# Performance work log

Hardware: AMD Instinct MI355X
Metric: run time of the kernel (lower is better)

Reference implementation:

```python
import jax, jax.numpy as jnp
import numpy as np

B, N, C = 8, 1024, 768
HEADS = 8
HD = C // HEADS  # head_dim = qk_dim // num_heads since qk_ratio=1
SCALE = HD ** (-0.5)


def setup_inputs() -> dict:
    key = jax.random.key(0)
    ks = jax.random.split(key, 8)
    s = 0.02
    return {
        "x": jax.random.normal(ks[0], (B, N, C), dtype=jnp.float32),
        "y": jax.random.normal(ks[1], (B, N, C), dtype=jnp.float32),
        "relative_pos": jax.random.normal(ks[2], (HEADS, N, N), dtype=jnp.float32),
        "H": 32,
        "W": 32,
        "Wq": jax.random.normal(ks[3], (C, C), dtype=jnp.float32) * s,
        "Wk": jax.random.normal(ks[4], (C, C), dtype=jnp.float32) * s,
        "Wv": jax.random.normal(ks[5], (C, C), dtype=jnp.float32) * s,
        "Wp": jax.random.normal(ks[6], (C, C), dtype=jnp.float32) * s,
        "bp": jnp.zeros((C,), dtype=jnp.float32),
    }


def reference(x, y, relative_pos, H, W, Wq, Wk, Wv, Wp, bp):
    # sr_ratio == 1 path: K/V come directly from y (no spatial reduction).
    b, n, c = x.shape
    q = (x @ Wq.T).reshape(b, n, HEADS, HD)       # bnhd
    k = (y @ Wk.T).reshape(b, n, HEADS, HD)       # bmhd
    v = (y @ Wv.T).reshape(b, n, HEADS, HD)       # bmhd
    # scores: QK^T * scale + learned relative position bias (broadcast over batch)
    attn = jnp.einsum("bnhd,bmhd->bhnm", q, k) * SCALE + relative_pos[None]
    attn = jax.nn.softmax(attn, axis=-1)
    out = jnp.einsum("bhnm,bmhd->bnhd", attn, v).reshape(b, n, c)
    return out @ Wp.T + bp
```

## Files before the change

kernel.cpp:

```cpp
#include <hip/hip_runtime.h>
#include <hip/hip_bf16.h>
#include <cstdint>
#include <cstddef>


using f32x4  = __attribute__((ext_vector_type(4))) float;
using bf16x8 = __attribute__((ext_vector_type(8))) __bf16;

constexpr int Bb = 8, Nn = 1024, Cc = 768;
constexpr float LOG2E = 1.4426950408889634f;
constexpr float QSC   = 0.10206207261596575f * 1.4426950408889634f;

__device__ __forceinline__ uint16_t f2bf(float f) {
  union { float f; uint32_t u; } v; v.f = f;
  return (uint16_t)((v.u + 0x7fffu + ((v.u >> 16) & 1u)) >> 16);
}

__device__ __forceinline__ void gl_lds16(const void* g, void* l) {
  __builtin_amdgcn_global_load_lds(
      (const __attribute__((address_space(1))) void*)g,
      (__attribute__((address_space(3))) void*)l, 16, 0, 0);
}

__device__ __forceinline__ f32x4 mfma16(bf16x8 a, bf16x8 b, f32x4 c) {
  return __builtin_amdgcn_mfma_f32_16x16x32_bf16(a, b, c, 0, 0, 0);
}

template <int CTRL>
__device__ __forceinline__ float dpp_add(float v) {
  union { float f; int i; } u, r;
  u.f = v;
  r.i = __builtin_amdgcn_update_dpp(u.i, u.i, CTRL, 0xF, 0xF, false);
  return v + r.f;
}
__device__ __forceinline__ float red16_add(float v) {
  v = dpp_add<0x128>(v);
  v = dpp_add<0x124>(v);
  v = dpp_add<0x122>(v);
  v = dpp_add<0x121>(v);
  return v;
}

constexpr int NX4 = (Bb * Nn * Cc) / 4;
constexpr int NW4 = (Cc * Cc) / 4;
__global__ void cvt_all(const float* __restrict__ x, const float* __restrict__ y,
                        const float* __restrict__ wq, const float* __restrict__ wk,
                        const float* __restrict__ wv, const float* __restrict__ wp,
                        uint16_t* __restrict__ xb, uint16_t* __restrict__ yb,
                        uint16_t* __restrict__ dq, uint16_t* __restrict__ dk,
                        uint16_t* __restrict__ dv, uint16_t* __restrict__ dp) {
  int i = blockIdx.x * blockDim.x + threadIdx.x;
  const float* s; uint16_t* d; int off; float sc = 1.f;
  if (i < NX4) {
    s = x; d = xb; off = i;
  } else if (i < 2 * NX4) {
    s = y; d = yb; off = i - NX4;
  } else {
    int j = i - 2 * NX4;
    int wsel = j / NW4;
    off = j - wsel * NW4;
    switch (wsel) {
      case 0:  s = wq; d = dq; sc = QSC; break;
      case 1:  s = wk; d = dk; break;
      case 2:  s = wv; d = dv; break;
      default: s = wp; d = dp; break;
    }
  }
  float4 v = ((const float4*)s)[off];
  ushort4 o;
  o.x = f2bf(v.x * sc); o.y = f2bf(v.y * sc);
  o.z = f2bf(v.z * sc); o.w = f2bf(v.w * sc);
  ((ushort4*)d)[off] = o;
}

__device__ __forceinline__ void gemm_core(const uint16_t* __restrict__ A,
                                          const uint16_t* __restrict__ Bt,
                                          uint16_t* As, uint16_t* Bs,
                                          int m0, int n0, f32x4 (&acc)[4][4]) {
  const int tid = threadIdx.x;
  const int lane = tid & 63, l16 = lane & 15, quad = lane >> 4;
  const int w = tid >> 6;
  const int wm = (w & 1) * 64, wn = (w >> 1) * 64;

  int soff[4];
#pragma unroll
  for (int i = 0; i < 4; ++i) {
    int idx = tid + 256 * i;
    int row = idx >> 3, pc = idx & 7;
    int c = pc ^ (row & 7);
    soff[i] = row * 768 + c * 8;
  }

  for (int k0 = 0; k0 < 768; k0 += 64) {
    __syncthreads();
#pragma unroll
    for (int i = 0; i < 4; ++i)
      gl_lds16(A + (size_t)m0 * 768 + k0 + soff[i], &As[(tid + 256 * i) * 8]);
#pragma unroll
    for (int i = 0; i < 4; ++i)
      gl_lds16(Bt + (size_t)n0 * 768 + k0 + soff[i], &Bs[(tid + 256 * i) * 8]);
    __syncthreads();

#pragma unroll
    for (int ks = 0; ks < 2; ++ks) {
      bf16x8 a[4], b[4];
      const int phys = (ks * 4 + quad) ^ (l16 & 7);
#pragma unroll
      for (int i = 0; i < 4; ++i)
        a[i] = *(const bf16x8*)&As[(wm + i * 16 + l16) * 64 + phys * 8];
#pragma unroll
      for (int j = 0; j < 4; ++j)
        b[j] = *(const bf16x8*)&Bs[(wn + j * 16 + l16) * 64 + phys * 8];
#pragma unroll
      for (int i = 0; i < 4; ++i)
#pragma unroll
        for (int j = 0; j < 4; ++j)
          acc[i][j] = mfma16(a[i], b[j], acc[i][j]);
    }
  }
}

__global__ __launch_bounds__(256, 3) void qkv_kernel(
    const uint16_t* __restrict__ xb, const uint16_t* __restrict__ yb,
    const uint16_t* __restrict__ wq, const uint16_t* __restrict__ wk,
    const uint16_t* __restrict__ wv, uint16_t* __restrict__ Qb,
    uint16_t* __restrict__ Kb, uint16_t* __restrict__ Vt) {
  __shared__ uint16_t smem[128 * 130];
  const int seg = blockIdx.x / 6, nb = blockIdx.x % 6;
  const uint16_t* A  = (seg == 0) ? xb : yb;
  const uint16_t* Bt = (seg == 0) ? wq : (seg == 1) ? wk : wv;
  const int m0 = blockIdx.y * 128, n0 = nb * 128;

  f32x4 acc[4][4] = {};
  gemm_core(A, Bt, smem, smem + 8192, m0, n0, acc);

  const int tid = threadIdx.x, lane = tid & 63;
  const int l16 = lane & 15, quad = lane >> 4, w = tid >> 6;
  const int wm = (w & 1) * 64, wn = (w >> 1) * 64;

  if (seg <= 1) {
    uint16_t* O = seg ? Kb : Qb;
#pragma unroll
    for (int i = 0; i < 4; ++i)
#pragma unroll
      for (int j = 0; j < 4; ++j) {
        int col = n0 + wn + j * 16 + l16;
#pragma unroll
        for (int r = 0; r < 4; ++r) {
          int row = m0 + wm + i * 16 + quad * 4 + r;
          O[(size_t)row * 768 + col] = f2bf(acc[i][j][r]);
        }
      }
  } else {
    __syncthreads();
#pragma unroll
    for (int i = 0; i < 4; ++i)
#pragma unroll
      for (int j = 0; j < 4; ++j) {
        int ml = wm + i * 16 + quad * 4;
        int nl = wn + j * 16 + l16;
        ushort4 pk;
        pk.x = f2bf(acc[i][j][0]); pk.y = f2bf(acc[i][j][1]);
        pk.z = f2bf(acc[i][j][2]); pk.w = f2bf(acc[i][j][3]);
        *(ushort4*)&smem[nl * 130 + ml] = pk;
      }
    __syncthreads();
    const int bidx = m0 >> 10, nseq0 = m0 & 1023;
#pragma unroll
    for (int pass = 0; pass < 8; ++pass) {
      int nl = pass * 16 + (tid >> 4);
      int col = n0 + nl;
      int h = col / 96, hd = col % 96;
      int m = (tid & 15) * 8;
      bf16x8 v = *(const bf16x8*)&smem[nl * 130 + m];
      size_t o = (((size_t)(bidx * 8 + h) * 96 + hd) << 10) + nseq0 + m;
      *(bf16x8*)(Vt + o) = v;
    }
  }
}

__global__ __launch_bounds__(256, 4) void proj_kernel(
    const uint16_t* __restrict__ A, const uint16_t* __restrict__ Bt,
    float* __restrict__ out, const float* __restrict__ bias) {
  __shared__ uint16_t As[64 * 64];
  __shared__ uint16_t Bs[128 * 64];
  const int m0 = blockIdx.y * 64, n0 = blockIdx.x * 128;
  const int tid = threadIdx.x, lane = tid & 63;
  const int l16 = lane & 15, quad = lane >> 4, w = tid >> 6;
  const int wm = (w & 1) * 32, wn = (w >> 1) * 64;

  int soffA[2], soffB[4];
#pragma unroll
  for (int i = 0; i < 2; ++i) {
    int idx = tid + 256 * i;
    int row = idx >> 3, pc = idx & 7;
    soffA[i] = row * 768 + (pc ^ (row & 7)) * 8;
  }
#pragma unroll
  for (int i = 0; i < 4; ++i) {
    int idx = tid + 256 * i;
    int row = idx >> 3, pc = idx & 7;
    soffB[i] = row * 768 + (pc ^ (row & 7)) * 8;
  }

  f32x4 acc[2][4] = {};
  for (int k0 = 0; k0 < 768; k0 += 64) {
    __syncthreads();
#pragma unroll
    for (int i = 0; i < 2; ++i)
      gl_lds16(A + (size_t)m0 * 768 + k0 + soffA[i], &As[(tid + 256 * i) * 8]);
#pragma unroll
    for (int i = 0; i < 4; ++i)
      gl_lds16(Bt + (size_t)n0 * 768 + k0 + soffB[i], &Bs[(tid + 256 * i) * 8]);
    __syncthreads();
#pragma unroll
    for (int ks = 0; ks < 2; ++ks) {
      bf16x8 a[2], b[4];
      const int phys = (ks * 4 + quad) ^ (l16 & 7);
#pragma unroll
      for (int i = 0; i < 2; ++i)
        a[i] = *(const bf16x8*)&As[(wm + i * 16 + l16) * 64 + phys * 8];
#pragma unroll
      for (int j = 0; j < 4; ++j)
        b[j] = *(const bf16x8*)&Bs[(wn + j * 16 + l16) * 64 + phys * 8];
#pragma unroll
      for (int i = 0; i < 2; ++i)
#pragma unroll
        for (int j = 0; j < 4; ++j)
          acc[i][j] = mfma16(a[i], b[j], acc[i][j]);
    }
  }

  float bv[4];
#pragma unroll
  for (int j = 0; j < 4; ++j) bv[j] = bias[n0 + wn + j * 16 + l16];
#pragma unroll
  for (int i = 0; i < 2; ++i)
#pragma unroll
    for (int j = 0; j < 4; ++j) {
      int col = n0 + wn + j * 16 + l16;
#pragma unroll
      for (int r = 0; r < 4; ++r) {
        int row = m0 + wm + i * 16 + quad * 4 + r;
        out[(size_t)row * 768 + col] = acc[i][j][r] + bv[j];
      }
    }
}

__global__ __launch_bounds__(256, 2) void attn_kernel(
    const uint16_t* __restrict__ Q,
    const uint16_t* __restrict__ Kb,
    const uint16_t* __restrict__ Vt,
    const float* __restrict__ rel,
    uint16_t* __restrict__ AO) {
  __shared__ uint16_t Ks[2][64 * 96];
  __shared__ uint16_t Vs[2][96 * 64];
  __shared__ uint16_t Ps[128 * 64];

  const int tid = threadIdx.x;
  const int q0 = blockIdx.x * 128;
  const int bh = blockIdx.y;
  const int b = bh >> 3, h = bh & 7;
  const int w = tid >> 6, lane = tid & 63;
  const int l16 = lane & 15, quad = lane >> 4;
  const int l7 = l16 & 7;

  bf16x8 qf[2][3];
#pragma unroll
  for (int st = 0; st < 2; ++st) {
    const int qrow = q0 + st * 64 + w * 16 + l16;
    const uint16_t* qp =
        Q + ((size_t)(b * 1024 + qrow)) * 768 + h * 96 + quad * 8;
#pragma unroll
    for (int j = 0; j < 3; ++j) qf[st][j] = *(const bf16x8*)(qp + j * 32);
  }

  auto kSrc = [](int c) {
    int r = c / 12, pc = c % 12;
    int kc = (pc < 8) ? (pc ^ (r & 7)) : (8 + ((pc & 3) ^ (r & 3)));
    return r * 768 + kc * 8;
  };
  auto vSrc = [](int c) {
    int d = c >> 3, pc = c & 7;
    return d * 1024 + (pc ^ (d & 7)) * 8;
  };
  int koffs[3], voffs[3];
#pragma unroll
  for (int i = 0; i < 3; ++i) {
    koffs[i] = kSrc(tid + 256 * i);
    voffs[i] = vSrc(tid + 256 * i);
  }

  const uint16_t* kslab = Kb + ((size_t)(b * 1024)) * 768 + h * 96;
  const uint16_t* vslab = Vt + ((size_t)(bh * 96) << 10);
  const float* relbase0 =
      rel + ((size_t)h << 20) + ((size_t)(q0 + w * 16 + quad * 4) << 10) + l16;
  const float* relbase1 = relbase0 + (64 << 10);

  auto stage = [&](int knext, int bufi) {
    const uint16_t* kb = kslab + (size_t)knext * 768;
    const uint16_t* vb = vslab + knext;
    uint16_t* Kbuf = &Ks[bufi][0];
    uint16_t* Vbuf = &Vs[bufi][0];
#pragma unroll
    for (int i = 0; i < 3; ++i) {
      gl_lds16(kb + koffs[i], Kbuf + (tid + 256 * i) * 8);
      gl_lds16(vb + voffs[i], Vbuf + (tid + 256 * i) * 8);
    }
  };

  float relv[2][16];
  auto loadrel = [&](int knext) {
#pragma unroll
    for (int r = 0; r < 4; ++r)
#pragma unroll
      for (int nt = 0; nt < 4; ++nt) {
        relv[0][nt * 4 + r] = relbase0[(size_t)r * 1024 + knext + nt * 16];
        relv[1][nt * 4 + r] = relbase1[(size_t)r * 1024 + knext + nt * 16];
      }
  };

  float l_i[2][4] = {};
  f32x4 o_acc[2][6] = {};

  stage(0, 0);
  loadrel(0);

#pragma unroll 2
  for (int kt = 0; kt < 16; ++kt) {
    const int cur = kt & 1, nxt = (kt + 1) & 1;
    __syncthreads();
    if (kt < 15) stage((kt + 1) * 64, nxt);
    const uint16_t* KsC = &Ks[cur][0];
    const uint16_t* VsC = &Vs[cur][0];

    f32x4 s[2][4] = {};
#pragma unroll
    for (int ksi = 0; ksi < 3; ++ksi) {
#pragma unroll
      for (int nt = 0; nt < 4; ++nt) {
        const int row = nt * 16 + l16;
        const int c = ksi * 4 + quad;
        const int phys =
            (ksi < 2) ? (c ^ (row & 7)) : (8 + ((c & 3) ^ (row & 3)));
        bf16x8 kf = *(const bf16x8*)&KsC[row * 96 + phys * 8];
        s[0][nt] = mfma16(qf[0][ksi], kf, s[0][nt]);
        s[1][nt] = mfma16(qf[1][ksi], kf, s[1][nt]);
      }
    }

    const int khi = l16 >> 3;
#pragma unroll
    for (int st = 0; st < 2; ++st) {
      float pv[16];
#pragma unroll
      for (int nt = 0; nt < 4; ++nt)
#pragma unroll
        for (int r = 0; r < 4; ++r)
          pv[nt * 4 + r] = __builtin_amdgcn_exp2f(
              fmaf(relv[st][nt * 4 + r], LOG2E, s[st][nt][r]));
#pragma unroll
      for (int r = 0; r < 4; ++r)
        l_i[st][r] += (pv[r] + pv[4 + r]) + (pv[8 + r] + pv[12 + r]);
#pragma unroll
      for (int r = 0; r < 4; ++r) {
        const int qloc = quad * 4 + r;
        const int rowoff = (st * 64 + w * 16 + qloc) * 64;
        const int sw = qloc & 7;
#pragma unroll
        for (int nt = 0; nt < 4; ++nt) {
          const int kc = 2 * nt + khi;
          Ps[rowoff + (((kc ^ sw) << 3) | l7)] = f2bf(pv[nt * 4 + r]);
        }
      }
    }

    if (kt < 15) loadrel((kt + 1) * 64);

    asm volatile("s_waitcnt lgkmcnt(0)" ::: "memory");

#pragma unroll
    for (int ksi = 0; ksi < 2; ++ksi) {
      const int phys = (ksi * 4 + quad) ^ l7;
      bf16x8 pf0 = *(const bf16x8*)&Ps[(w * 16 + l16) * 64 + phys * 8];
      bf16x8 pf1 = *(const bf16x8*)&Ps[(64 + w * 16 + l16) * 64 + phys * 8];
#pragma unroll
      for (int jt = 0; jt < 6; ++jt) {
        const int d = jt * 16 + l16;
        bf16x8 vf = *(const bf16x8*)&VsC[d * 64 + phys * 8];
        o_acc[0][jt] = mfma16(pf0, vf, o_acc[0][jt]);
        o_acc[1][jt] = mfma16(pf1, vf, o_acc[1][jt]);
      }
    }
  }

#pragma unroll
  for (int st = 0; st < 2; ++st)
#pragma unroll
    for (int r = 0; r < 4; ++r) {
      float inv = 1.f / red16_add(l_i[st][r]);
      int row = q0 + st * 64 + w * 16 + quad * 4 + r;
#pragma unroll
      for (int jt = 0; jt < 6; ++jt) {
        int col = h * 96 + jt * 16 + l16;
        AO[(size_t)(b * 1024 + row) * 768 + col] = f2bf(o_acc[st][jt][r] * inv);
      }
    }
}

extern "C" void kernel_launch(void* const* d_in, const int* in_sizes, int n_in,
                              void* d_out, int out_size, void* d_ws,
                              size_t ws_size, hipStream_t stream) {
  const float* x   = (const float*)d_in[0];
  const float* y   = (const float*)d_in[1];
  const float* rel = (const float*)d_in[2];
  const float* Wq  = (const float*)d_in[5];
  const float* Wk  = (const float*)d_in[6];
  const float* Wv  = (const float*)d_in[7];
  const float* Wp  = (const float*)d_in[8];
  const float* bp  = (const float*)d_in[9];
  float* out = (float*)d_out;

  const size_t nBNC = (size_t)Bb * Nn * Cc;
  const size_t nW = (size_t)Cc * Cc;

  char* ws = (char*)d_ws;
  size_t off = 0;
  auto alloc = [&](size_t bytes) {
    char* p = ws + off;
    off += (bytes + 255) & ~(size_t)255;
    return p;
  };
  uint16_t* xb  = (uint16_t*)alloc(nBNC * 2);
  uint16_t* yb  = (uint16_t*)alloc(nBNC * 2);
  uint16_t* wqb = (uint16_t*)alloc(nW * 2);
  uint16_t* wkb = (uint16_t*)alloc(nW * 2);
  uint16_t* wvb = (uint16_t*)alloc(nW * 2);
  uint16_t* wpb = (uint16_t*)alloc(nW * 2);
  uint16_t* Qb  = (uint16_t*)alloc(nBNC * 2);
  uint16_t* Kb  = (uint16_t*)alloc(nBNC * 2);
  uint16_t* Vtb = (uint16_t*)alloc(nBNC * 2);
  uint16_t* AOb = (uint16_t*)alloc(nBNC * 2);

  const int cvtBlocks = (2 * NX4 + 4 * NW4) / 256;
  cvt_all<<<cvtBlocks, 256, 0, stream>>>(x, y, Wq, Wk, Wv, Wp, xb, yb, wqb,
                                         wkb, wvb, wpb);

  qkv_kernel<<<dim3(18, 64), 256, 0, stream>>>(xb, yb, wqb, wkb, wvb, Qb, Kb,
                                               Vtb);

  attn_kernel<<<dim3(8, 64), 256, 0, stream>>>(Qb, Kb, Vtb, rel, AOb);

  proj_kernel<<<dim3(6, 128), 256, 0, stream>>>(AOb, wpb, out, bp);
}
```

Baseline: 239.3 us.

## Use 8 waves per attention block and swizzle block order across heads

The attention kernel goes from 4 waves that each own two 16-row query strips to 8 waves that each own one strip, so each thread keeps half as many accumulators and the K/V staging load is split across 512 threads. The grid becomes one-dimensional with a swizzled block index that groups blocks sharing the same relative-position head, aiming for better L2 reuse of the bias tensor. The intent is higher occupancy and latency hiding from lower register pressure. In exchange, each wave reuses every K/V fragment read from LDS for only one MFMA instead of two, and the larger blocks make barriers costlier.

```diff
diff --git a/kernel.cpp b/kernel.cpp
--- a/kernel.cpp
+++ b/kernel.cpp
@@ -247,7 +247,7 @@
     }
 }
 
-__global__ __launch_bounds__(256, 2) void attn_kernel(
+__global__ __launch_bounds__(512, 4) void attn_kernel(
     const uint16_t* __restrict__ Q,
     const uint16_t* __restrict__ Kb,
     const uint16_t* __restrict__ Vt,
@@ -258,21 +258,24 @@
   __shared__ uint16_t Ps[128 * 64];
 
   const int tid = threadIdx.x;
-  const int q0 = blockIdx.x * 128;
-  const int bh = blockIdx.y;
-  const int b = bh >> 3, h = bh & 7;
+  const int id = blockIdx.x;
+  const int swz = (id & 7) * 64 + (id >> 3);
+  const int h  = swz >> 6;
+  const int q0 = ((swz >> 3) & 7) * 128;
+  const int b  = swz & 7;
+  const int bh = b * 8 + h;
+
   const int w = tid >> 6, lane = tid & 63;
   const int l16 = lane & 15, quad = lane >> 4;
   const int l7 = l16 & 7;
 
-  bf16x8 qf[2][3];
-#pragma unroll
-  for (int st = 0; st < 2; ++st) {
-    const int qrow = q0 + st * 64 + w * 16 + l16;
+  bf16x8 qf[3];
+  {
+    const int qrow = q0 + w * 16 + l16;
     const uint16_t* qp =
         Q + ((size_t)(b * 1024 + qrow)) * 768 + h * 96 + quad * 8;
 #pragma unroll
-    for (int j = 0; j < 3; ++j) qf[st][j] = *(const bf16x8*)(qp + j * 32);
+    for (int j = 0; j < 3; ++j) qf[j] = *(const bf16x8*)(qp + j * 32);
   }
 
   auto kSrc = [](int c) {
@@ -284,44 +287,42 @@
     int d = c >> 3, pc = c & 7;
     return d * 1024 + (pc ^ (d & 7)) * 8;
   };
-  int koffs[3], voffs[3];
+  int soff[3], ldst[3]; bool isK[3];
 #pragma unroll
   for (int i = 0; i < 3; ++i) {
-    koffs[i] = kSrc(tid + 256 * i);
-    voffs[i] = vSrc(tid + 256 * i);
+    int idx = tid + 512 * i;
+    isK[i] = idx < 768;
+    int c = isK[i] ? idx : idx - 768;
+    soff[i] = isK[i] ? kSrc(c) : vSrc(c);
+    ldst[i] = c * 8;
   }
 
   const uint16_t* kslab = Kb + ((size_t)(b * 1024)) * 768 + h * 96;
   const uint16_t* vslab = Vt + ((size_t)(bh * 96) << 10);
-  const float* relbase0 =
+  const float* relbase =
       rel + ((size_t)h << 20) + ((size_t)(q0 + w * 16 + quad * 4) << 10) + l16;
-  const float* relbase1 = relbase0 + (64 << 10);
 
   auto stage = [&](int knext, int bufi) {
     const uint16_t* kb = kslab + (size_t)knext * 768;
     const uint16_t* vb = vslab + knext;
-    uint16_t* Kbuf = &Ks[bufi][0];
-    uint16_t* Vbuf = &Vs[bufi][0];
 #pragma unroll
     for (int i = 0; i < 3; ++i) {
-      gl_lds16(kb + koffs[i], Kbuf + (tid + 256 * i) * 8);
-      gl_lds16(vb + voffs[i], Vbuf + (tid + 256 * i) * 8);
+      if (isK[i]) gl_lds16(kb + soff[i], &Ks[bufi][ldst[i]]);
+      else        gl_lds16(vb + soff[i], &Vs[bufi][ldst[i]]);
     }
   };
 
-  float relv[2][16];
+  float relv[16];
   auto loadrel = [&](int knext) {
 #pragma unroll
     for (int r = 0; r < 4; ++r)
 #pragma unroll
-      for (int nt = 0; nt < 4; ++nt) {
-        relv[0][nt * 4 + r] = relbase0[(size_t)r * 1024 + knext + nt * 16];
-        relv[1][nt * 4 + r] = relbase1[(size_t)r * 1024 + knext + nt * 16];
-      }
+      for (int nt = 0; nt < 4; ++nt)
+        relv[nt * 4 + r] = relbase[(size_t)r * 1024 + knext + nt * 16];
   };
 
-  float l_i[2][4] = {};
-  f32x4 o_acc[2][6] = {};
+  float l_i[4] = {};
+  f32x4 o_acc[6] = {};
 
   stage(0, 0);
   loadrel(0);
@@ -334,7 +335,7 @@
     const uint16_t* KsC = &Ks[cur][0];
     const uint16_t* VsC = &Vs[cur][0];
 
-    f32x4 s[2][4] = {};
+    f32x4 s[4] = {};
 #pragma unroll
     for (int ksi = 0; ksi < 3; ++ksi) {
 #pragma unroll
@@ -344,34 +345,30 @@
         const int phys =
             (ksi < 2) ? (c ^ (row & 7)) : (8 + ((c & 3) ^ (row & 3)));
         bf16x8 kf = *(const bf16x8*)&KsC[row * 96 + phys * 8];
-        s[0][nt] = mfma16(qf[0][ksi], kf, s[0][nt]);
-        s[1][nt] = mfma16(qf[1][ksi], kf, s[1][nt]);
+        s[nt] = mfma16(qf[ksi], kf, s[nt]);
       }
     }
 
     const int khi = l16 >> 3;
-#pragma unroll
-    for (int st = 0; st < 2; ++st) {
-      float pv[16];
-#pragma unroll
-      for (int nt = 0; nt < 4; ++nt)
-#pragma unroll
-        for (int r = 0; r < 4; ++r)
-          pv[nt * 4 + r] = __builtin_amdgcn_exp2f(
-              fmaf(relv[st][nt * 4 + r], LOG2E, s[st][nt][r]));
+    float pv[16];
+#pragma unroll
+    for (int nt = 0; nt < 4; ++nt)
 #pragma unroll
       for (int r = 0; r < 4; ++r)
-        l_i[st][r] += (pv[r] + pv[4 + r]) + (pv[8 + r] + pv[12 + r]);
-#pragma unroll
-      for (int r = 0; r < 4; ++r) {
-        const int qloc = quad * 4 + r;
-        const int rowoff = (st * 64 + w * 16 + qloc) * 64;
-        const int sw = qloc & 7;
-#pragma unroll
-        for (int nt = 0; nt < 4; ++nt) {
-          const int kc = 2 * nt + khi;
-          Ps[rowoff + (((kc ^ sw) << 3) | l7)] = f2bf(pv[nt * 4 + r]);
-        }
+        pv[nt * 4 + r] = __builtin_amdgcn_exp2f(
+            fmaf(relv[nt * 4 + r], LOG2E, s[nt][r]));
+#pragma unroll
+    for (int r = 0; r < 4; ++r)
+      l_i[r] += (pv[r] + pv[4 + r]) + (pv[8 + r] + pv[12 + r]);
+#pragma unroll
+    for (int r = 0; r < 4; ++r) {
+      const int qloc = quad * 4 + r;
+      const int rowoff = (w * 16 + qloc) * 64;
+      const int sw = qloc & 7;
+#pragma unroll
+      for (int nt = 0; nt < 4; ++nt) {
+        const int kc = 2 * nt + khi;
+        Ps[rowoff + (((kc ^ sw) << 3) | l7)] = f2bf(pv[nt * 4 + r]);
       }
     }
 
@@ -382,30 +379,26 @@
 #pragma unroll
     for (int ksi = 0; ksi < 2; ++ksi) {
       const int phys = (ksi * 4 + quad) ^ l7;
-      bf16x8 pf0 = *(const bf16x8*)&Ps[(w * 16 + l16) * 64 + phys * 8];
-      bf16x8 pf1 = *(const bf16x8*)&Ps[(64 + w * 16 + l16) * 64 + phys * 8];
+      bf16x8 pf = *(const bf16x8*)&Ps[(w * 16 + l16) * 64 + phys * 8];
 #pragma unroll
       for (int jt = 0; jt < 6; ++jt) {
         const int d = jt * 16 + l16;
         bf16x8 vf = *(const bf16x8*)&VsC[d * 64 + phys * 8];
-        o_acc[0][jt] = mfma16(pf0, vf, o_acc[0][jt]);
-        o_acc[1][jt] = mfma16(pf1, vf, o_acc[1][jt]);
-      }
-    }
-  }
-
-#pragma unroll
-  for (int st = 0; st < 2; ++st)
-#pragma unroll
-    for (int r = 0; r < 4; ++r) {
-      float inv = 1.f / red16_add(l_i[st][r]);
-      int row = q0 + st * 64 + w * 16 + quad * 4 + r;
-#pragma unroll
-      for (int jt = 0; jt < 6; ++jt) {
-        int col = h * 96 + jt * 16 + l16;
-        AO[(size_t)(b * 1024 + row) * 768 + col] = f2bf(o_acc[st][jt][r] * inv);
-      }
-    }
+        o_acc[jt] = mfma16(pf, vf, o_acc[jt]);
+      }
+    }
+  }
+
+#pragma unroll
+  for (int r = 0; r < 4; ++r) {
+    float inv = 1.f / red16_add(l_i[r]);
+    int row = q0 + w * 16 + quad * 4 + r;
+#pragma unroll
+    for (int jt = 0; jt < 6; ++jt) {
+      int col = h * 96 + jt * 16 + l16;
+      AO[(size_t)(b * 1024 + row) * 768 + col] = f2bf(o_acc[jt][r] * inv);
+    }
+  }
 }
 
 extern "C" void kernel_launch(void* const* d_in, const int* in_sizes, int n_in,
@@ -449,7 +442,7 @@
   qkv_kernel<<<dim3(18, 64), 256, 0, stream>>>(xb, yb, wqb, wkb, wvb, Qb, Kb,
                                                Vtb);
 
-  attn_kernel<<<dim3(8, 64), 256, 0, stream>>>(Qb, Kb, Vtb, rel, AOb);
+  attn_kernel<<<dim3(512), 512, 0, stream>>>(Qb, Kb, Vtb, rel, AOb);
 
   proj_kernel<<<dim3(6, 128), 256, 0, stream>>>(AOb, wpb, out, bp);
 }
```

Result: slower. 259.3 us (+8.3%).

## Split attention key tiles across two wave groups with LDS reduction

Applied to the files above, without the earlier changes.

Raises the attention block from 4 to 8 waves. Each group of 4 waves handles half of every 64-key tile for QK, softmax and PV, and the two partial accumulators are combined through shared memory at the end. The grid also becomes 1D with a swizzled block-to-(b,h,q) mapping, which changes the launch order. The aim is more waves in flight to hide latency and fewer registers per wave. The cost is an extra end-of-kernel LDS reduction and a reduced PV K-dimension per wave.

```diff
diff --git a/kernel.cpp b/kernel.cpp
--- a/kernel.cpp
+++ b/kernel.cpp
@@ -247,28 +247,34 @@
     }
 }
 
-__global__ __launch_bounds__(256, 2) void attn_kernel(
+__global__ __launch_bounds__(512, 4) void attn_kernel(
     const uint16_t* __restrict__ Q,
     const uint16_t* __restrict__ Kb,
     const uint16_t* __restrict__ Vt,
     const float* __restrict__ rel,
     uint16_t* __restrict__ AO) {
-  __shared__ uint16_t Ks[2][64 * 96];
-  __shared__ uint16_t Vs[2][96 * 64];
-  __shared__ uint16_t Ps[128 * 64];
+  __shared__ uint16_t smem[32768];
+  uint16_t* KsB = smem;
+  uint16_t* VsB = smem + 12288;
+  uint16_t* Ps  = smem + 24576;
 
   const int tid = threadIdx.x;
-  const int q0 = blockIdx.x * 128;
-  const int bh = blockIdx.y;
-  const int b = bh >> 3, h = bh & 7;
+  const int id = blockIdx.x;
+  const int swz = (id & 7) * 64 + (id >> 3);
+  const int h  = swz >> 6;
+  const int q0 = ((swz >> 3) & 7) * 128;
+  const int b  = swz & 7;
+  const int bh = b * 8 + h;
+
   const int w = tid >> 6, lane = tid & 63;
+  const int w2 = w & 3, khalf = w >> 2;
   const int l16 = lane & 15, quad = lane >> 4;
   const int l7 = l16 & 7;
 
   bf16x8 qf[2][3];
 #pragma unroll
   for (int st = 0; st < 2; ++st) {
-    const int qrow = q0 + st * 64 + w * 16 + l16;
+    const int qrow = q0 + st * 64 + w2 * 16 + l16;
     const uint16_t* qp =
         Q + ((size_t)(b * 1024 + qrow)) * 768 + h * 96 + quad * 8;
 #pragma unroll
@@ -284,37 +290,41 @@
     int d = c >> 3, pc = c & 7;
     return d * 1024 + (pc ^ (d & 7)) * 8;
   };
-  int koffs[3], voffs[3];
+  int soff[3], ldst[3]; bool isK[3];
 #pragma unroll
   for (int i = 0; i < 3; ++i) {
-    koffs[i] = kSrc(tid + 256 * i);
-    voffs[i] = vSrc(tid + 256 * i);
+    int idx = tid + 512 * i;
+    isK[i] = idx < 768;
+    int c = isK[i] ? idx : idx - 768;
+    soff[i] = isK[i] ? kSrc(c) : vSrc(c);
+    ldst[i] = c * 8;
   }
 
   const uint16_t* kslab = Kb + ((size_t)(b * 1024)) * 768 + h * 96;
   const uint16_t* vslab = Vt + ((size_t)(bh * 96) << 10);
-  const float* relbase0 =
-      rel + ((size_t)h << 20) + ((size_t)(q0 + w * 16 + quad * 4) << 10) + l16;
+  const float* relbase0 = rel + ((size_t)h << 20) +
+                          ((size_t)(q0 + w2 * 16 + quad * 4) << 10) +
+                          khalf * 32 + l16;
   const float* relbase1 = relbase0 + (64 << 10);
 
   auto stage = [&](int knext, int bufi) {
     const uint16_t* kb = kslab + (size_t)knext * 768;
     const uint16_t* vb = vslab + knext;
-    uint16_t* Kbuf = &Ks[bufi][0];
-    uint16_t* Vbuf = &Vs[bufi][0];
+    uint16_t* Kbuf = KsB + bufi * 6144;
+    uint16_t* Vbuf = VsB + bufi * 6144;
 #pragma unroll
     for (int i = 0; i < 3; ++i) {
-      gl_lds16(kb + koffs[i], Kbuf + (tid + 256 * i) * 8);
-      gl_lds16(vb + voffs[i], Vbuf + (tid + 256 * i) * 8);
+      if (isK[i]) gl_lds16(kb + soff[i], Kbuf + ldst[i]);
+      else        gl_lds16(vb + soff[i], Vbuf + ldst[i]);
     }
   };
 
-  float relv[2][16];
+  float relv[2][8];
   auto loadrel = [&](int knext) {
 #pragma unroll
     for (int r = 0; r < 4; ++r)
 #pragma unroll
-      for (int nt = 0; nt < 4; ++nt) {
+      for (int nt = 0; nt < 2; ++nt) {
         relv[0][nt * 4 + r] = relbase0[(size_t)r * 1024 + knext + nt * 16];
         relv[1][nt * 4 + r] = relbase1[(size_t)r * 1024 + knext + nt * 16];
       }
@@ -331,15 +341,15 @@
     const int cur = kt & 1, nxt = (kt + 1) & 1;
     __syncthreads();
     if (kt < 15) stage((kt + 1) * 64, nxt);
-    const uint16_t* KsC = &Ks[cur][0];
-    const uint16_t* VsC = &Vs[cur][0];
-
-    f32x4 s[2][4] = {};
+    const uint16_t* KsC = KsB + cur * 6144;
+    const uint16_t* VsC = VsB + cur * 6144;
+
+    f32x4 s[2][2] = {};
 #pragma unroll
     for (int ksi = 0; ksi < 3; ++ksi) {
 #pragma unroll
-      for (int nt = 0; nt < 4; ++nt) {
-        const int row = nt * 16 + l16;
+      for (int nt = 0; nt < 2; ++nt) {
+        const int row = (khalf * 2 + nt) * 16 + l16;
         const int c = ksi * 4 + quad;
         const int phys =
             (ksi < 2) ? (c ^ (row & 7)) : (8 + ((c & 3) ^ (row & 3)));
@@ -352,25 +362,25 @@
     const int khi = l16 >> 3;
 #pragma unroll
     for (int st = 0; st < 2; ++st) {
-      float pv[16];
-#pragma unroll
-      for (int nt = 0; nt < 4; ++nt)
+      float pv[8];
+#pragma unroll
+      for (int nt = 0; nt < 2; ++nt)
 #pragma unroll
         for (int r = 0; r < 4; ++r)
           pv[nt * 4 + r] = __builtin_amdgcn_exp2f(
               fmaf(relv[st][nt * 4 + r], LOG2E, s[st][nt][r]));
 #pragma unroll
       for (int r = 0; r < 4; ++r)
-        l_i[st][r] += (pv[r] + pv[4 + r]) + (pv[8 + r] + pv[12 + r]);
+        l_i[st][r] += pv[r] + pv[4 + r];
 #pragma unroll
       for (int r = 0; r < 4; ++r) {
         const int qloc = quad * 4 + r;
-        const int rowoff = (st * 64 + w * 16 + qloc) * 64;
+        const int rowoff = (st * 64 + w2 * 16 + qloc) * 64;
         const int sw = qloc & 7;
 #pragma unroll
-        for (int nt = 0; nt < 4; ++nt) {
-          const int kc = 2 * nt + khi;
-          Ps[rowoff + (((kc ^ sw) << 3) | l7)] = f2bf(pv[nt * 4 + r]);
+        for (int nt = 0; nt < 2; ++nt) {
+          const int kcg = (khalf * 2 + nt) * 2 + khi;
+          Ps[rowoff + (((kcg ^ sw) << 3) | l7)] = f2bf(pv[nt * 4 + r]);
         }
       }
     }
@@ -379,11 +389,10 @@
 
     asm volatile("s_waitcnt lgkmcnt(0)" ::: "memory");
 
-#pragma unroll
-    for (int ksi = 0; ksi < 2; ++ksi) {
-      const int phys = (ksi * 4 + quad) ^ l7;
-      bf16x8 pf0 = *(const bf16x8*)&Ps[(w * 16 + l16) * 64 + phys * 8];
-      bf16x8 pf1 = *(const bf16x8*)&Ps[(64 + w * 16 + l16) * 64 + phys * 8];
+    {
+      const int phys = (khalf * 4 + quad) ^ l7;
+      bf16x8 pf0 = *(const bf16x8*)&Ps[(w2 * 16 + l16) * 64 + phys * 8];
+      bf16x8 pf1 = *(const bf16x8*)&Ps[(64 + w2 * 16 + l16) * 64 + phys * 8];
 #pragma unroll
       for (int jt = 0; jt < 6; ++jt) {
         const int d = jt * 16 + l16;
@@ -394,18 +403,43 @@
     }
   }
 
-#pragma unroll
-  for (int st = 0; st < 2; ++st)
-#pragma unroll
-    for (int r = 0; r < 4; ++r) {
-      float inv = 1.f / red16_add(l_i[st][r]);
-      int row = q0 + st * 64 + w * 16 + quad * 4 + r;
-#pragma unroll
-      for (int jt = 0; jt < 6; ++jt) {
-        int col = h * 96 + jt * 16 + l16;
-        AO[(size_t)(b * 1024 + row) * 768 + col] = f2bf(o_acc[st][jt][r] * inv);
-      }
-    }
+  __syncthreads();
+  float* red = (float*)smem;
+  float* pr = red + (w2 * 3840 + lane * 60);
+  if (khalf) {
+#pragma unroll
+    for (int st = 0; st < 2; ++st) {
+#pragma unroll
+      for (int jt = 0; jt < 6; ++jt)
+        *(f32x4*)&pr[(st * 6 + jt) * 4] = o_acc[st][jt];
+#pragma unroll
+      for (int r = 0; r < 4; ++r) pr[48 + st * 4 + r] = l_i[st][r];
+    }
+  }
+  __syncthreads();
+  if (!khalf) {
+#pragma unroll
+    for (int st = 0; st < 2; ++st) {
+#pragma unroll
+      for (int jt = 0; jt < 6; ++jt)
+        o_acc[st][jt] += *(const f32x4*)&pr[(st * 6 + jt) * 4];
+#pragma unroll
+      for (int r = 0; r < 4; ++r) l_i[st][r] += pr[48 + st * 4 + r];
+    }
+#pragma unroll
+    for (int st = 0; st < 2; ++st)
+#pragma unroll
+      for (int r = 0; r < 4; ++r) {
+        float inv = 1.f / red16_add(l_i[st][r]);
+        int row = q0 + st * 64 + w2 * 16 + quad * 4 + r;
+#pragma unroll
+        for (int jt = 0; jt < 6; ++jt) {
+          int col = h * 96 + jt * 16 + l16;
+          AO[(size_t)(b * 1024 + row) * 768 + col] =
+              f2bf(o_acc[st][jt][r] * inv);
+        }
+      }
+  }
 }
 
 extern "C" void kernel_launch(void* const* d_in, const int* in_sizes, int n_in,
@@ -449,7 +483,7 @@
   qkv_kernel<<<dim3(18, 64), 256, 0, stream>>>(xb, yb, wqb, wkb, wvb, Qb, Kb,
                                                Vtb);
 
-  attn_kernel<<<dim3(8, 64), 256, 0, stream>>>(Qb, Kb, Vtb, rel, AOb);
+  attn_kernel<<<dim3(512), 512, 0, stream>>>(Qb, Kb, Vtb, rel, AOb);
 
   proj_kernel<<<dim3(6, 128), 256, 0, stream>>>(AOb, wpb, out, bp);
 }
```

Measured after the change: 428.2 us. 79.0% more time.

## Fuse K and V projections per block and swizzle block order across XCDs

Applied to the files above, without the earlier changes.

The QKV kernel now computes K and V together in one block, loading each y tile once and multiplying it against both Wk and Wv. This halves the A-tile traffic for those projections but doubles the accumulator registers, so the occupancy bound drops from 3 to 2. All three kernels now use 1D grids with an XCD-aware remapping, so blocks on the same XCD share M tiles or heads for better L2 reuse. The grid shrinks from 1152 to 768 qkv blocks, and the work per block becomes uneven: Q blocks do one GEMM while K/V blocks do two.

```diff
diff --git a/kernel.cpp b/kernel.cpp
--- a/kernel.cpp
+++ b/kernel.cpp
@@ -120,26 +120,26 @@
   }
 }
 
-__global__ __launch_bounds__(256, 3) void qkv_kernel(
+__global__ __launch_bounds__(256, 2) void qkv_kernel(
     const uint16_t* __restrict__ xb, const uint16_t* __restrict__ yb,
     const uint16_t* __restrict__ wq, const uint16_t* __restrict__ wk,
     const uint16_t* __restrict__ wv, uint16_t* __restrict__ Qb,
     uint16_t* __restrict__ Kb, uint16_t* __restrict__ Vt) {
-  __shared__ uint16_t smem[128 * 130];
-  const int seg = blockIdx.x / 6, nb = blockIdx.x % 6;
-  const uint16_t* A  = (seg == 0) ? xb : yb;
-  const uint16_t* Bt = (seg == 0) ? wq : (seg == 1) ? wk : wv;
-  const int m0 = blockIdx.y * 128, n0 = nb * 128;
-
-  f32x4 acc[4][4] = {};
-  gemm_core(A, Bt, smem, smem + 8192, m0, n0, acc);
+  __shared__ uint16_t smem[24576];
+  const int id = blockIdx.x;
+  const int xcd = id & 7, jj = id >> 3;
+  const int mt = xcd * 8 + (jj & 7);
+  const int rest = jj >> 3;
+  const int kind = rest / 6, nb = rest % 6;
+  const int m0 = mt * 128, n0 = nb * 128;
 
   const int tid = threadIdx.x, lane = tid & 63;
   const int l16 = lane & 15, quad = lane >> 4, w = tid >> 6;
   const int wm = (w & 1) * 64, wn = (w >> 1) * 64;
 
-  if (seg <= 1) {
-    uint16_t* O = seg ? Kb : Qb;
+  if (kind == 0) {
+    f32x4 acc[4][4] = {};
+    gemm_core(xb, wq, smem, smem + 8192, m0, n0, acc);
 #pragma unroll
     for (int i = 0; i < 4; ++i)
 #pragma unroll
@@ -148,34 +148,95 @@
 #pragma unroll
         for (int r = 0; r < 4; ++r) {
           int row = m0 + wm + i * 16 + quad * 4 + r;
-          O[(size_t)row * 768 + col] = f2bf(acc[i][j][r]);
+          Qb[(size_t)row * 768 + col] = f2bf(acc[i][j][r]);
         }
       }
-  } else {
-    __syncthreads();
-#pragma unroll
-    for (int i = 0; i < 4; ++i)
+    return;
+  }
+
+  uint16_t* As = smem;
+  uint16_t* Bk = smem + 8192;
+  uint16_t* Bv = smem + 16384;
+
+  int soff[4];
+#pragma unroll
+  for (int i = 0; i < 4; ++i) {
+    int idx = tid + 256 * i;
+    int row = idx >> 3, pc = idx & 7;
+    soff[i] = row * 768 + (pc ^ (row & 7)) * 8;
+  }
+
+  f32x4 ak[4][4] = {}, av[4][4] = {};
+  for (int k0 = 0; k0 < 768; k0 += 64) {
+    __syncthreads();
+#pragma unroll
+    for (int i = 0; i < 4; ++i)
+      gl_lds16(yb + (size_t)m0 * 768 + k0 + soff[i], &As[(tid + 256 * i) * 8]);
+#pragma unroll
+    for (int i = 0; i < 4; ++i)
+      gl_lds16(wk + (size_t)n0 * 768 + k0 + soff[i], &Bk[(tid + 256 * i) * 8]);
+#pragma unroll
+    for (int i = 0; i < 4; ++i)
+      gl_lds16(wv + (size_t)n0 * 768 + k0 + soff[i], &Bv[(tid + 256 * i) * 8]);
+    __syncthreads();
+
+#pragma unroll
+    for (int ks = 0; ks < 2; ++ks) {
+      bf16x8 a[4], bk[4], bv[4];
+      const int phys = (ks * 4 + quad) ^ (l16 & 7);
+#pragma unroll
+      for (int i = 0; i < 4; ++i)
+        a[i] = *(const bf16x8*)&As[(wm + i * 16 + l16) * 64 + phys * 8];
 #pragma unroll
       for (int j = 0; j < 4; ++j) {
-        int ml = wm + i * 16 + quad * 4;
-        int nl = wn + j * 16 + l16;
-        ushort4 pk;
-        pk.x = f2bf(acc[i][j][0]); pk.y = f2bf(acc[i][j][1]);
-        pk.z = f2bf(acc[i][j][2]); pk.w = f2bf(acc[i][j][3]);
-        *(ushort4*)&smem[nl * 130 + ml] = pk;
-      }
-    __syncthreads();
-    const int bidx = m0 >> 10, nseq0 = m0 & 1023;
-#pragma unroll
-    for (int pass = 0; pass < 8; ++pass) {
-      int nl = pass * 16 + (tid >> 4);
-      int col = n0 + nl;
-      int h = col / 96, hd = col % 96;
-      int m = (tid & 15) * 8;
-      bf16x8 v = *(const bf16x8*)&smem[nl * 130 + m];
-      size_t o = (((size_t)(bidx * 8 + h) * 96 + hd) << 10) + nseq0 + m;
-      *(bf16x8*)(Vt + o) = v;
-    }
+        bk[j] = *(const bf16x8*)&Bk[(wn + j * 16 + l16) * 64 + phys * 8];
+        bv[j] = *(const bf16x8*)&Bv[(wn + j * 16 + l16) * 64 + phys * 8];
+      }
+#pragma unroll
+      for (int i = 0; i < 4; ++i)
+#pragma unroll
+        for (int j = 0; j < 4; ++j) {
+          ak[i][j] = mfma16(a[i], bk[j], ak[i][j]);
+          av[i][j] = mfma16(a[i], bv[j], av[i][j]);
+        }
+    }
+  }
+
+#pragma unroll
+  for (int i = 0; i < 4; ++i)
+#pragma unroll
+    for (int j = 0; j < 4; ++j) {
+      int col = n0 + wn + j * 16 + l16;
+#pragma unroll
+      for (int r = 0; r < 4; ++r) {
+        int row = m0 + wm + i * 16 + quad * 4 + r;
+        Kb[(size_t)row * 768 + col] = f2bf(ak[i][j][r]);
+      }
+    }
+
+  __syncthreads();
+#pragma unroll
+  for (int i = 0; i < 4; ++i)
+#pragma unroll
+    for (int j = 0; j < 4; ++j) {
+      int ml = wm + i * 16 + quad * 4;
+      int nl = wn + j * 16 + l16;
+      ushort4 pk;
+      pk.x = f2bf(av[i][j][0]); pk.y = f2bf(av[i][j][1]);
+      pk.z = f2bf(av[i][j][2]); pk.w = f2bf(av[i][j][3]);
+      *(ushort4*)&smem[nl * 130 + ml] = pk;
+    }
+  __syncthreads();
+  const int bidx = m0 >> 10, nseq0 = m0 & 1023;
+#pragma unroll
+  for (int pass = 0; pass < 8; ++pass) {
+    int nl = pass * 16 + (tid >> 4);
+    int col = n0 + nl;
+    int h = col / 96, hd = col % 96;
+    int m = (tid & 15) * 8;
+    bf16x8 v = *(const bf16x8*)&smem[nl * 130 + m];
+    size_t o = (((size_t)(bidx * 8 + h) * 96 + hd) << 10) + nseq0 + m;
+    *(bf16x8*)(Vt + o) = v;
   }
 }
 
@@ -184,7 +245,11 @@
     float* __restrict__ out, const float* __restrict__ bias) {
   __shared__ uint16_t As[64 * 64];
   __shared__ uint16_t Bs[128 * 64];
-  const int m0 = blockIdx.y * 64, n0 = blockIdx.x * 128;
+  const int id = blockIdx.x;
+  const int xcd = id & 7, jj = id >> 3;
+  const int mt = xcd * 16 + (jj & 15);
+  const int nb = jj >> 4;
+  const int m0 = mt * 64, n0 = nb * 128;
   const int tid = threadIdx.x, lane = tid & 63;
   const int l16 = lane & 15, quad = lane >> 4, w = tid >> 6;
   const int wm = (w & 1) * 32, wn = (w >> 1) * 64;
@@ -258,9 +323,13 @@
   __shared__ uint16_t Ps[128 * 64];
 
   const int tid = threadIdx.x;
-  const int q0 = blockIdx.x * 128;
-  const int bh = blockIdx.y;
-  const int b = bh >> 3, h = bh & 7;
+  const int id = blockIdx.x;
+  const int swz = (id & 7) * 64 + (id >> 3);
+  const int h  = swz >> 6;
+  const int q0 = ((swz >> 3) & 7) * 128;
+  const int b  = swz & 7;
+  const int bh = b * 8 + h;
+
   const int w = tid >> 6, lane = tid & 63;
   const int l16 = lane & 15, quad = lane >> 4;
   const int l7 = l16 & 7;
@@ -446,10 +515,10 @@
   cvt_all<<<cvtBlocks, 256, 0, stream>>>(x, y, Wq, Wk, Wv, Wp, xb, yb, wqb,
                                          wkb, wvb, wpb);
 
-  qkv_kernel<<<dim3(18, 64), 256, 0, stream>>>(xb, yb, wqb, wkb, wvb, Qb, Kb,
-                                               Vtb);
-
-  attn_kernel<<<dim3(8, 64), 256, 0, stream>>>(Qb, Kb, Vtb, rel, AOb);
-
-  proj_kernel<<<dim3(6, 128), 256, 0, stream>>>(AOb, wpb, out, bp);
-}
+  qkv_kernel<<<dim3(768), 256, 0, stream>>>(xb, yb, wqb, wkb, wvb, Qb, Kb,
+                                            Vtb);
+
+  attn_kernel<<<dim3(512), 256, 0, stream>>>(Qb, Kb, Vtb, rel, AOb);
+
+  proj_kernel<<<dim3(768), 256, 0, stream>>>(AOb, wpb, out, bp);
+}
```

Result: no change. 235.8 us (-1.5%).
